# Kernel optimization log

Measured on AMD Instinct MI355X. Metric: run time of the kernel, lower is better.

Reference implementation:

```python
import jax, jax.numpy as jnp
import numpy as np

N_VAR = 16384   # variable nodes N
N_CHK = 8192    # check nodes M
N_EDGE = 65536  # edges E (avg variable degree 4)
BATCH = 1024
LLR_CLIP = 15.0
EPS = 1e-6
# clamp floor for |lam| in H_Step: -log(tanh(llr_clip/2))
ABS_MIN = np.float32(-np.log(np.tanh(LLR_CLIP / 2.0)))


def _atanh(x):
    x = x * (1.0 - EPS)
    return 0.5 * jnp.log((1.0 + x) / (1.0 - x))


def setup_inputs() -> dict:
    key = jax.random.key(0)
    ks = jax.random.split(key, 7)
    chn_llr = jax.random.normal(ks[0], (N_VAR, BATCH), dtype=jnp.float32) * 3.0
    msg_C2V = jax.random.normal(ks[1], (N_EDGE, BATCH), dtype=jnp.float32)
    msg_V2C = jax.random.normal(ks[2], (N_EDGE, BATCH), dtype=jnp.float32)
    # Wi, We ~ N(mean=1, std=0.001) per 'simple' mode init
    Wi = 1.0 + 0.001 * jax.random.normal(ks[3], (1,), dtype=jnp.float32)
    We = 1.0 + 0.001 * jax.random.normal(ks[4], (1,), dtype=jnp.float32)
    gamma = jnp.full((1,), 0.9, dtype=jnp.float32)
    var_idx = jax.random.randint(ks[5], (N_EDGE,), 0, N_VAR, dtype=jnp.int32)
    chk_idx = jax.random.randint(ks[6], (N_EDGE,), 0, N_CHK, dtype=jnp.int32)
    return {"chn_llr": chn_llr, "msg_C2V": msg_C2V, "msg_V2C": msg_V2C,
            "Wi": Wi, "We": We, "gamma": gamma,
            "var_idx": var_idx, "chk_idx": chk_idx}


def _bp_forward(chn_llr, msg_C2V, msg_V2C, Wi, We, gamma, var_idx, chk_idx):
    def col_sum(x):  # (E,B) -> (N,B)
        return jax.ops.segment_sum(x, var_idx, num_segments=N_VAR)

    def col_sum_loo(x):  # leave-one-out over edges of same variable
        return col_sum(x)[var_idx] - x

    def row_sum_loo(x):  # leave-one-out over edges of same check
        return jax.ops.segment_sum(x, chk_idx, num_segments=N_CHK)[chk_idx] - x

    # ---- V step: V2C messages ----
    ell_w, lam_w = Wi * chn_llr, We * msg_C2V
    v_new = ell_w[var_idx] + col_sum_loo(lam_w)           # (E,B)
    msg_V2C = (1.0 - gamma) * msg_V2C + gamma * v_new     # damping

    # ---- H step: C2V messages ----
    lam = jnp.clip(msg_V2C, -LLR_CLIP, LLR_CLIP)
    neg = (lam < 0).astype(lam.dtype)
    cnt = row_sum_loo(neg)
    sgn = 1.0 - 2.0 * jnp.mod(cnt, 2.0)                   # == (-1)**cnt
    abs_lam = jnp.clip(jnp.abs(lam), ABS_MIN, LLR_CLIP)
    amp = row_sum_loo(jnp.log(jnp.tanh(abs_lam / 2.0)))
    h_new = jax.lax.stop_gradient(sgn) * 2.0 * _atanh(jnp.exp(amp))
    msg_C2V = (1.0 - gamma) * msg_C2V + gamma * h_new     # damping

    # ---- M step: marginals ----
    output = Wi * chn_llr + col_sum(We * msg_C2V)         # (N,B)
    return msg_C2V, msg_V2C, output


def reference(chn_llr, msg_C2V, msg_V2C, Wi, We, gamma, var_idx, chk_idx):
    return _bp_forward(chn_llr, msg_C2V, msg_V2C, Wi, We, gamma, var_idx, chk_idx)
```

## Files before the change

kernel.cpp:

```cpp
#include <hip/hip_runtime.h>
#include <cstdint>
#include <cstddef>

#define N_VAR  16384
#define N_CHK  8192
#define N_EDGE 65536
#define BATCH  1024

static constexpr float LLR_CLIP = 15.0f;
static constexpr float ABS_MIN_F = 6.1180464e-7f;
static constexpr float EPS1 = 0.999999f;

__device__ __forceinline__ float4 ld4(const float* __restrict__ p, int row, int t) {
    return ((const float4*)(p + (size_t)row * BATCH))[t];
}
__device__ __forceinline__ void st4(float* __restrict__ p, int row, int t, float4 v) {
    ((float4*)(p + (size_t)row * BATCH))[t] = v;
}

__device__ __forceinline__ float loglam_f(float nv, float& neg) {
    float lam = fminf(fmaxf(nv, -LLR_CLIP), LLR_CLIP);
    neg = (lam < 0.0f) ? 1.0f : 0.0f;
    float a = fminf(fmaxf(fabsf(lam), ABS_MIN_F), LLR_CLIP);
    float t = __expf(-a);
    return __logf((1.0f - t) / (1.0f + t));
}

__global__ __launch_bounds__(256) void hist_k(const int* __restrict__ vi, const int* __restrict__ ci,
                                              int* __restrict__ vcnt, int* __restrict__ ccnt) {
    int e = blockIdx.x * 256 + threadIdx.x;
    if (e < N_EDGE) {
        atomicAdd(&vcnt[vi[e]], 1);
        atomicAdd(&ccnt[ci[e]], 1);
    }
}

template <int PER>
__global__ __launch_bounds__(1024) void scan_k(int* __restrict__ cnt, int* __restrict__ ptr) {
    __shared__ int sdata[1024];
    const int n = PER * 1024;
    int t = threadIdx.x;
    int base = t * PER;
    int loc[PER];
    int sum = 0;
#pragma unroll
    for (int i = 0; i < PER; i++) { loc[i] = sum; sum += cnt[base + i]; }
    sdata[t] = sum;
    __syncthreads();
    for (int off = 1; off < 1024; off <<= 1) {
        int v = (t >= off) ? sdata[t - off] : 0;
        __syncthreads();
        sdata[t] += v;
        __syncthreads();
    }
    int excl = (t == 0) ? 0 : sdata[t - 1];
#pragma unroll
    for (int i = 0; i < PER; i++) {
        int p = excl + loc[i];
        ptr[base + i] = p;
        cnt[base + i] = p;
    }
    if (t == 1023) ptr[n] = sdata[1023];
}

__global__ __launch_bounds__(256) void scatter_k(const int* __restrict__ vi, const int* __restrict__ ci,
                                                 int* __restrict__ vcur, int* __restrict__ ccur,
                                                 int* __restrict__ vedg, int* __restrict__ cedg) {
    int e = blockIdx.x * 256 + threadIdx.x;
    if (e < N_EDGE) {
        int p = atomicAdd(&vcur[vi[e]], 1); vedg[p] = e;
        int q = atomicAdd(&ccur[ci[e]], 1); cedg[q] = e;
    }
}

__global__ __launch_bounds__(256) void k1_var_acc(const float* __restrict__ chn,
                                                  const float* __restrict__ c2v,
                                                  const float* __restrict__ Wi_p,
                                                  const float* __restrict__ We_p,
                                                  const int* __restrict__ vptr,
                                                  const int* __restrict__ vedg,
                                                  float* __restrict__ acc_v) {
    int v = blockIdx.x, t = threadIdx.x;
    float Wi = Wi_p[0], We = We_p[0];
    float4 a = ld4(chn, v, t);
    a.x *= Wi; a.y *= Wi; a.z *= Wi; a.w *= Wi;
    int s = vptr[v], e1 = vptr[v + 1];
    for (int i = s; i < e1; i++) {
        int e = vedg[i];
        float4 m = ld4(c2v, e, t);
        a.x += We * m.x; a.y += We * m.y; a.z += We * m.z; a.w += We * m.w;
    }
    st4(acc_v, v, t, a);
}

__global__ __launch_bounds__(256) void k2_chk(const float* __restrict__ c2v,
                                              const float* __restrict__ v2c,
                                              const float* __restrict__ acc_v,
                                              const float* __restrict__ We_p,
                                              const float* __restrict__ g_p,
                                              const int* __restrict__ cptr,
                                              const int* __restrict__ cedg,
                                              const int* __restrict__ vi,
                                              float* __restrict__ out_v2c,
                                              float* __restrict__ acc_cnt,
                                              float* __restrict__ acc_amp) {
    int c = blockIdx.x, t = threadIdx.x;
    float We = We_p[0], g = g_p[0], gm = 1.0f - g;
    float4 cnt = make_float4(0.f, 0.f, 0.f, 0.f);
    float4 amp = make_float4(0.f, 0.f, 0.f, 0.f);
    int s = cptr[c], e1 = cptr[c + 1];
    for (int i = s; i < e1; i++) {
        int e = cedg[i];
        int v = vi[e];
        float4 m  = ld4(c2v, e, t);
        float4 p  = ld4(v2c, e, t);
        float4 av = ld4(acc_v, v, t);
        float4 nv;
        nv.x = gm * p.x + g * (av.x - We * m.x);
        nv.y = gm * p.y + g * (av.y - We * m.y);
        nv.z = gm * p.z + g * (av.z - We * m.z);
        nv.w = gm * p.w + g * (av.w - We * m.w);
        st4(out_v2c, e, t, nv);
        float ng;
        float ll;
        ll = loglam_f(nv.x, ng); cnt.x += ng; amp.x += ll;
        ll = loglam_f(nv.y, ng); cnt.y += ng; amp.y += ll;
        ll = loglam_f(nv.z, ng); cnt.z += ng; amp.z += ll;
        ll = loglam_f(nv.w, ng); cnt.w += ng; amp.w += ll;
    }
    st4(acc_cnt, c, t, cnt);
    st4(acc_amp, c, t, amp);
}

__global__ __launch_bounds__(256) void k3_var_out(const float* __restrict__ chn,
                                                  const float* __restrict__ c2v,
                                                  const float* __restrict__ v2c_new,
                                                  const float* __restrict__ acc_cnt,
                                                  const float* __restrict__ acc_amp,
                                                  const float* __restrict__ Wi_p,
                                                  const float* __restrict__ We_p,
                                                  const float* __restrict__ g_p,
                                                  const int* __restrict__ vptr,
                                                  const int* __restrict__ vedg,
                                                  const int* __restrict__ ci,
                                                  float* __restrict__ out_c2v,
                                                  float* __restrict__ out_marg) {
    int v = blockIdx.x, t = threadIdx.x;
    float Wi = Wi_p[0], We = We_p[0], g = g_p[0], gm = 1.0f - g;
    float4 ch = ld4(chn, v, t);
    float4 osum;
    osum.x = Wi * ch.x; osum.y = Wi * ch.y; osum.z = Wi * ch.z; osum.w = Wi * ch.w;
    int s = vptr[v], e1 = vptr[v + 1];
    for (int i = s; i < e1; i++) {
        int e = vedg[i];
        int c = ci[e];
        float4 nv = ld4(v2c_new, e, t);
        float4 tc = ld4(acc_cnt, c, t);
        float4 ta = ld4(acc_amp, c, t);
        float4 m  = ld4(c2v, e, t);
        float4 cn;
        {
            float ng; float ll = loglam_f(nv.x, ng);
            float cl = tc.x - ng;
            float al = fminf(ta.x - ll, 0.0f);
            float sg = (((int)(cl + 0.5f)) & 1) ? -1.0f : 1.0f;
            float x0 = __expf(al) * EPS1;
            float h  = sg * __logf((1.0f + x0) / (1.0f - x0));
            cn.x = gm * m.x + g * h;
            osum.x += We * cn.x;
        }
        {
            float ng; float ll = loglam_f(nv.y, ng);
            float cl = tc.y - ng;
            float al = fminf(ta.y - ll, 0.0f);
            float sg = (((int)(cl + 0.5f)) & 1) ? -1.0f : 1.0f;
            float x0 = __expf(al) * EPS1;
            float h  = sg * __logf((1.0f + x0) / (1.0f - x0));
            cn.y = gm * m.y + g * h;
            osum.y += We * cn.y;
        }
        {
            float ng; float ll = loglam_f(nv.z, ng);
            float cl = tc.z - ng;
            float al = fminf(ta.z - ll, 0.0f);
            float sg = (((int)(cl + 0.5f)) & 1) ? -1.0f : 1.0f;
            float x0 = __expf(al) * EPS1;
            float h  = sg * __logf((1.0f + x0) / (1.0f - x0));
            cn.z = gm * m.z + g * h;
            osum.z += We * cn.z;
        }
        {
            float ng; float ll = loglam_f(nv.w, ng);
            float cl = tc.w - ng;
            float al = fminf(ta.w - ll, 0.0f);
            float sg = (((int)(cl + 0.5f)) & 1) ? -1.0f : 1.0f;
            float x0 = __expf(al) * EPS1;
            float h  = sg * __logf((1.0f + x0) / (1.0f - x0));
            cn.w = gm * m.w + g * h;
            osum.w += We * cn.w;
        }
        st4(out_c2v, e, t, cn);
    }
    st4(out_marg, v, t, osum);
}

extern "C" void kernel_launch(void* const* d_in, const int* in_sizes, int n_in,
                              void* d_out, int out_size, void* d_ws, size_t ws_size,
                              hipStream_t stream) {
    const float* chn   = (const float*)d_in[0];
    const float* c2v   = (const float*)d_in[1];
    const float* v2c   = (const float*)d_in[2];
    const float* Wi_p  = (const float*)d_in[3];
    const float* We_p  = (const float*)d_in[4];
    const float* g_p   = (const float*)d_in[5];
    const int*   vi    = (const int*)d_in[6];
    const int*   ci    = (const int*)d_in[7];

    float* out_c2v  = (float*)d_out;
    float* out_v2c  = out_c2v + (size_t)N_EDGE * BATCH;
    float* out_marg = out_v2c + (size_t)N_EDGE * BATCH;
    float* acc_v    = out_marg;

    float* acc_cnt = (float*)d_ws;
    float* acc_amp = acc_cnt + (size_t)N_CHK * BATCH;
    int*   iws     = (int*)(acc_amp + (size_t)N_CHK * BATCH);
    int*   vcnt = iws;
    int*   ccnt = vcnt + N_VAR;
    int*   vptr = ccnt + N_CHK;
    int*   cptr = vptr + (N_VAR + 1);
    int*   vedg = cptr + (N_CHK + 1);
    int*   cedg = vedg + N_EDGE;

    hipMemsetAsync(vcnt, 0, (size_t)(N_VAR + N_CHK) * sizeof(int), stream);
    hist_k<<<N_EDGE / 256, 256, 0, stream>>>(vi, ci, vcnt, ccnt);
    scan_k<N_VAR / 1024><<<1, 1024, 0, stream>>>(vcnt, vptr);
    scan_k<N_CHK / 1024><<<1, 1024, 0, stream>>>(ccnt, cptr);
    scatter_k<<<N_EDGE / 256, 256, 0, stream>>>(vi, ci, vcnt, ccnt, vedg, cedg);

    k1_var_acc<<<N_VAR, 256, 0, stream>>>(chn, c2v, Wi_p, We_p, vptr, vedg, acc_v);
    k2_chk<<<N_CHK, 256, 0, stream>>>(c2v, v2c, acc_v, We_p, g_p, cptr, cedg, vi,
                                      out_v2c, acc_cnt, acc_amp);
    k3_var_out<<<N_VAR, 256, 0, stream>>>(chn, c2v, out_v2c, acc_cnt, acc_amp,
                                          Wi_p, We_p, g_p, vptr, vedg, ci,
                                          out_c2v, out_marg);
}
```

Baseline: 1.246 ms.

## Fuse check-node H step into check kernel and reuse var-acc for marginals

```diff
diff --git a/kernel.cpp b/kernel.cpp
--- a/kernel.cpp
+++ b/kernel.cpp
@@ -24,6 +24,17 @@
     float a = fminf(fmaxf(fabsf(lam), ABS_MIN_F), LLR_CLIP);
     float t = __expf(-a);
     return __logf((1.0f - t) / (1.0f + t));
+}
+
+__device__ __forceinline__ float hstep(float nv, float cntT, float ampT,
+                                       float gm, float g, float m) {
+    float ng; float ll = loglam_f(nv, ng);
+    float cl = cntT - ng;
+    float al = fminf(ampT - ll, 0.0f);
+    float sg = (((int)(cl + 0.5f)) & 1) ? -1.0f : 1.0f;
+    float x0 = __expf(al) * EPS1;
+    float h  = sg * __logf((1.0f + x0) / (1.0f - x0));
+    return gm * m + g * h;
 }
 
 __global__ __launch_bounds__(256) void hist_k(const int* __restrict__ vi, const int* __restrict__ ci,
@@ -65,143 +76,80 @@
 
 __global__ __launch_bounds__(256) void scatter_k(const int* __restrict__ vi, const int* __restrict__ ci,
                                                  int* __restrict__ vcur, int* __restrict__ ccur,
-                                                 int* __restrict__ vedg, int* __restrict__ cedg) {
+                                                 int* __restrict__ vedg, int2* __restrict__ cedg2) {
     int e = blockIdx.x * 256 + threadIdx.x;
     if (e < N_EDGE) {
-        int p = atomicAdd(&vcur[vi[e]], 1); vedg[p] = e;
-        int q = atomicAdd(&ccur[ci[e]], 1); cedg[q] = e;
+        int v = vi[e];
+        int p = atomicAdd(&vcur[v], 1);    vedg[p] = e;
+        int q = atomicAdd(&ccur[ci[e]], 1); cedg2[q] = make_int2(e, v);
     }
 }
 
-__global__ __launch_bounds__(256) void k1_var_acc(const float* __restrict__ chn,
-                                                  const float* __restrict__ c2v,
-                                                  const float* __restrict__ Wi_p,
-                                                  const float* __restrict__ We_p,
-                                                  const int* __restrict__ vptr,
-                                                  const int* __restrict__ vedg,
-                                                  float* __restrict__ acc_v) {
+__global__ __launch_bounds__(256) void k_var_acc(const float* __restrict__ chn,
+                                                 const float* __restrict__ msg,
+                                                 const float* __restrict__ Wi_p,
+                                                 const float* __restrict__ We_p,
+                                                 const int* __restrict__ vptr,
+                                                 const int* __restrict__ vedg,
+                                                 float* __restrict__ out) {
     int v = blockIdx.x, t = threadIdx.x;
     float Wi = Wi_p[0], We = We_p[0];
     float4 a = ld4(chn, v, t);
     a.x *= Wi; a.y *= Wi; a.z *= Wi; a.w *= Wi;
     int s = vptr[v], e1 = vptr[v + 1];
+#pragma unroll 2
     for (int i = s; i < e1; i++) {
         int e = vedg[i];
-        float4 m = ld4(c2v, e, t);
+        float4 m = ld4(msg, e, t);
         a.x += We * m.x; a.y += We * m.y; a.z += We * m.z; a.w += We * m.w;
     }
-    st4(acc_v, v, t, a);
+    st4(out, v, t, a);
 }
 
-__global__ __launch_bounds__(256) void k2_chk(const float* __restrict__ c2v,
-                                              const float* __restrict__ v2c,
-                                              const float* __restrict__ acc_v,
-                                              const float* __restrict__ We_p,
-                                              const float* __restrict__ g_p,
-                                              const int* __restrict__ cptr,
-                                              const int* __restrict__ cedg,
-                                              const int* __restrict__ vi,
-                                              float* __restrict__ out_v2c,
-                                              float* __restrict__ acc_cnt,
-                                              float* __restrict__ acc_amp) {
+__global__ __launch_bounds__(256) void k2_fused(const float* __restrict__ c2v,
+                                                const float* __restrict__ v2c,
+                                                const float* __restrict__ acc_v,
+                                                const float* __restrict__ We_p,
+                                                const float* __restrict__ g_p,
+                                                const int* __restrict__ cptr,
+                                                const int2* __restrict__ cedg2,
+                                                float* __restrict__ out_v2c,
+                                                float* __restrict__ out_c2v) {
     int c = blockIdx.x, t = threadIdx.x;
     float We = We_p[0], g = g_p[0], gm = 1.0f - g;
     float4 cnt = make_float4(0.f, 0.f, 0.f, 0.f);
     float4 amp = make_float4(0.f, 0.f, 0.f, 0.f);
     int s = cptr[c], e1 = cptr[c + 1];
+#pragma unroll 2
     for (int i = s; i < e1; i++) {
-        int e = cedg[i];
-        int v = vi[e];
-        float4 m  = ld4(c2v, e, t);
-        float4 p  = ld4(v2c, e, t);
-        float4 av = ld4(acc_v, v, t);
+        int2 ev = cedg2[i];
+        float4 m  = ld4(c2v, ev.x, t);
+        float4 p  = ld4(v2c, ev.x, t);
+        float4 av = ld4(acc_v, ev.y, t);
         float4 nv;
         nv.x = gm * p.x + g * (av.x - We * m.x);
         nv.y = gm * p.y + g * (av.y - We * m.y);
         nv.z = gm * p.z + g * (av.z - We * m.z);
         nv.w = gm * p.w + g * (av.w - We * m.w);
-        st4(out_v2c, e, t, nv);
-        float ng;
-        float ll;
+        st4(out_v2c, ev.x, t, nv);
+        float ng, ll;
         ll = loglam_f(nv.x, ng); cnt.x += ng; amp.x += ll;
         ll = loglam_f(nv.y, ng); cnt.y += ng; amp.y += ll;
         ll = loglam_f(nv.z, ng); cnt.z += ng; amp.z += ll;
         ll = loglam_f(nv.w, ng); cnt.w += ng; amp.w += ll;
     }
-    st4(acc_cnt, c, t, cnt);
-    st4(acc_amp, c, t, amp);
-}
-
-__global__ __launch_bounds__(256) void k3_var_out(const float* __restrict__ chn,
-                                                  const float* __restrict__ c2v,
-                                                  const float* __restrict__ v2c_new,
-                                                  const float* __restrict__ acc_cnt,
-                                                  const float* __restrict__ acc_amp,
-                                                  const float* __restrict__ Wi_p,
-                                                  const float* __restrict__ We_p,
-                                                  const float* __restrict__ g_p,
-                                                  const int* __restrict__ vptr,
-                                                  const int* __restrict__ vedg,
-                                                  const int* __restrict__ ci,
-                                                  float* __restrict__ out_c2v,
-                                                  float* __restrict__ out_marg) {
-    int v = blockIdx.x, t = threadIdx.x;
-    float Wi = Wi_p[0], We = We_p[0], g = g_p[0], gm = 1.0f - g;
-    float4 ch = ld4(chn, v, t);
-    float4 osum;
-    osum.x = Wi * ch.x; osum.y = Wi * ch.y; osum.z = Wi * ch.z; osum.w = Wi * ch.w;
-    int s = vptr[v], e1 = vptr[v + 1];
+#pragma unroll 2
     for (int i = s; i < e1; i++) {
-        int e = vedg[i];
-        int c = ci[e];
-        float4 nv = ld4(v2c_new, e, t);
-        float4 tc = ld4(acc_cnt, c, t);
-        float4 ta = ld4(acc_amp, c, t);
+        int e = cedg2[i].x;
+        float4 nv = ld4(out_v2c, e, t);
         float4 m  = ld4(c2v, e, t);
         float4 cn;
-        {
-            float ng; float ll = loglam_f(nv.x, ng);
-            float cl = tc.x - ng;
-            float al = fminf(ta.x - ll, 0.0f);
-            float sg = (((int)(cl + 0.5f)) & 1) ? -1.0f : 1.0f;
-            float x0 = __expf(al) * EPS1;
-            float h  = sg * __logf((1.0f + x0) / (1.0f - x0));
-            cn.x = gm * m.x + g * h;
-            osum.x += We * cn.x;
-        }
-        {
-            float ng; float ll = loglam_f(nv.y, ng);
-            float cl = tc.y - ng;
-            float al = fminf(ta.y - ll, 0.0f);
-            float sg = (((int)(cl + 0.5f)) & 1) ? -1.0f : 1.0f;
-            float x0 = __expf(al) * EPS1;
-            float h  = sg * __logf((1.0f + x0) / (1.0f - x0));
-            cn.y = gm * m.y + g * h;
-            osum.y += We * cn.y;
-        }
-        {
-            float ng; float ll = loglam_f(nv.z, ng);
-            float cl = tc.z - ng;
-            float al = fminf(ta.z - ll, 0.0f);
-            float sg = (((int)(cl + 0.5f)) & 1) ? -1.0f : 1.0f;
-            float x0 = __expf(al) * EPS1;
-            float h  = sg * __logf((1.0f + x0) / (1.0f - x0));
-            cn.z = gm * m.z + g * h;
-            osum.z += We * cn.z;
-        }
-        {
-            float ng; float ll = loglam_f(nv.w, ng);
-            float cl = tc.w - ng;
-            float al = fminf(ta.w - ll, 0.0f);
-            float sg = (((int)(cl + 0.5f)) & 1) ? -1.0f : 1.0f;
-            float x0 = __expf(al) * EPS1;
-            float h  = sg * __logf((1.0f + x0) / (1.0f - x0));
-            cn.w = gm * m.w + g * h;
-            osum.w += We * cn.w;
-        }
+        cn.x = hstep(nv.x, cnt.x, amp.x, gm, g, m.x);
+        cn.y = hstep(nv.y, cnt.y, amp.y, gm, g, m.y);
+        cn.z = hstep(nv.z, cnt.z, amp.z, gm, g, m.z);
+        cn.w = hstep(nv.w, cnt.w, amp.w, gm, g, m.w);
         st4(out_c2v, e, t, cn);
     }
-    st4(out_marg, v, t, osum);
 }
 
 extern "C" void kernel_launch(void* const* d_in, const int* in_sizes, int n_in,
@@ -221,26 +169,22 @@
     float* out_marg = out_v2c + (size_t)N_EDGE * BATCH;
     float* acc_v    = out_marg;
 
-    float* acc_cnt = (float*)d_ws;
-    float* acc_amp = acc_cnt + (size_t)N_CHK * BATCH;
-    int*   iws     = (int*)(acc_amp + (size_t)N_CHK * BATCH);
-    int*   vcnt = iws;
-    int*   ccnt = vcnt + N_VAR;
-    int*   vptr = ccnt + N_CHK;
-    int*   cptr = vptr + (N_VAR + 1);
-    int*   vedg = cptr + (N_CHK + 1);
-    int*   cedg = vedg + N_EDGE;
+    int*  iws   = (int*)d_ws;
+    int*  vcnt  = iws;
+    int*  ccnt  = vcnt + N_VAR;
+    int*  vptr  = ccnt + N_CHK;
+    int*  cptr  = vptr + (N_VAR + 1);
+    int*  vedg  = cptr + (N_CHK + 1);
+    int2* cedg2 = (int2*)(vedg + N_EDGE);
 
     hipMemsetAsync(vcnt, 0, (size_t)(N_VAR + N_CHK) * sizeof(int), stream);
     hist_k<<<N_EDGE / 256, 256, 0, stream>>>(vi, ci, vcnt, ccnt);
     scan_k<N_VAR / 1024><<<1, 1024, 0, stream>>>(vcnt, vptr);
     scan_k<N_CHK / 1024><<<1, 1024, 0, stream>>>(ccnt, cptr);
-    scatter_k<<<N_EDGE / 256, 256, 0, stream>>>(vi, ci, vcnt, ccnt, vedg, cedg);
+    scatter_k<<<N_EDGE / 256, 256, 0, stream>>>(vi, ci, vcnt, ccnt, vedg, cedg2);
 
-    k1_var_acc<<<N_VAR, 256, 0, stream>>>(chn, c2v, Wi_p, We_p, vptr, vedg, acc_v);
-    k2_chk<<<N_CHK, 256, 0, stream>>>(c2v, v2c, acc_v, We_p, g_p, cptr, cedg, vi,
-                                      out_v2c, acc_cnt, acc_amp);
-    k3_var_out<<<N_VAR, 256, 0, stream>>>(chn, c2v, out_v2c, acc_cnt, acc_amp,
-                                          Wi_p, We_p, g_p, vptr, vedg, ci,
-                                          out_c2v, out_marg);
+    k_var_acc<<<N_VAR, 256, 0, stream>>>(chn, c2v, Wi_p, We_p, vptr, vedg, acc_v);
+    k2_fused<<<N_CHK, 256, 0, stream>>>(c2v, v2c, acc_v, We_p, g_p, cptr, cedg2,
+                                        out_v2c, out_c2v);
+    k_var_acc<<<N_VAR, 256, 0, stream>>>(chn, out_c2v, Wi_p, We_p, vptr, vedg, out_marg);
 }
```

Measured after the change: 1.213 ms. -2.6%, faster.
